# Kernel optimization log

Hardware: AMD Instinct MI355X
Metric: run time of the kernel (lower is better)

The kernel has to match this reference:

```python
import jax, jax.numpy as jnp
import numpy as np

B, N = 16384, 20
NODE_D, EDGE_D, TIME_D = 172, 172, 100
H = 2
OUT_D = NODE_D + TIME_D          # 272, pad_dim == 0
KEY_D = NODE_D + EDGE_D + TIME_D  # 444
HD = OUT_D // H                   # 136
LN_EPS = 1e-5


def setup_inputs() -> dict:
    key = jax.random.key(0)
    ks = jax.random.split(key, 12)
    s = lambda fan_in: 1.0 / np.sqrt(fan_in)
    return {
        "node_feat": jax.random.normal(ks[0], (B, NODE_D), jnp.float32),
        "time_feat": jax.random.normal(ks[1], (B, 1, TIME_D), jnp.float32),
        "nbr_node_feat": jax.random.normal(ks[2], (B, N, NODE_D), jnp.float32),
        "nbr_time_feat": jax.random.normal(ks[3], (B, N, TIME_D), jnp.float32),
        "nbr_edge_feat": jax.random.normal(ks[4], (B, N, EDGE_D), jnp.float32),
        "nbr_mask": jax.random.randint(ks[5], (B, N), 0, 2, jnp.int32),
        # linear weights, torch convention [out, in]
        "W_Q": jax.random.uniform(ks[6], (OUT_D, OUT_D), jnp.float32, -s(OUT_D), s(OUT_D)),
        "W_K": jax.random.uniform(ks[7], (OUT_D, KEY_D), jnp.float32, -s(KEY_D), s(KEY_D)),
        "W_V": jax.random.uniform(ks[8], (OUT_D, KEY_D), jnp.float32, -s(KEY_D), s(KEY_D)),
        "W_O": jax.random.uniform(ks[9], (OUT_D, OUT_D), jnp.float32, -s(OUT_D), s(OUT_D)),
        "b_O": jax.random.uniform(ks[10], (OUT_D,), jnp.float32, -s(OUT_D), s(OUT_D)),
        "ln_g": jnp.ones((OUT_D,), jnp.float32),
        "ln_b": jnp.zeros((OUT_D,), jnp.float32),
    }


def reference(node_feat, time_feat, nbr_node_feat, nbr_time_feat, nbr_edge_feat,
              nbr_mask, W_Q, W_K, W_V, W_O, b_O, ln_g, ln_b):
    # query: [B,1,OUT_D] = cat(node_feat, time_feat)
    q_in = jnp.concatenate([node_feat[:, None, :], time_feat], axis=2)
    residual = q_in
    # key/value input: [B,N,KEY_D]
    kv_in = jnp.concatenate([nbr_node_feat, nbr_edge_feat, nbr_time_feat], axis=2)

    Q = (q_in @ W_Q.T).reshape(B, 1, H, HD)   # bqhd
    K = (kv_in @ W_K.T).reshape(B, N, H, HD)  # bnhd
    V = (kv_in @ W_V.T).reshape(B, N, H, HD)

    scores = jnp.einsum('bqhd,bnhd->bhqn', Q, K) * (HD ** -0.5)  # [B,H,1,N]
    mask = (nbr_mask == 0)[:, None, None, :]                      # [B,1,1,N]
    scores = jnp.where(mask, jnp.float32(-1e10), scores)
    A = jax.nn.softmax(scores, axis=-1)  # dropout is identity (eval)

    O = jnp.einsum('bhqn,bnhd->bqhd', A, V).reshape(B, 1, OUT_D)
    out = O @ W_O.T + b_O
    x = out + residual
    mu = jnp.mean(x, axis=-1, keepdims=True)
    var = jnp.mean(jnp.square(x - mu), axis=-1, keepdims=True)
    x = (x - mu) * jax.lax.rsqrt(var + LN_EPS) * ln_g + ln_b
    return x[:, 0, :]  # [B, OUT_D]
```

## Files before the change

kernel.cpp:

```cpp
#include <hip/hip_runtime.h>


namespace {
constexpr int kB = 16384;
constexpr int kN = 20;
constexpr float kScale = 0.08574929257125441f;
constexpr float kLnEps = 1e-5f;

constexpr size_t kOffMsw = 0;
constexpr size_t kOffPsw = kOffMsw + 516096;
constexpr size_t kOffQT16 = kOffPsw + 487424;

constexpr int kMswBlocks = 56 * 9 * 8;
constexpr int kPswBlocks = 17 * 28 * 8;
}

typedef __attribute__((ext_vector_type(8))) short s8v;
typedef __attribute__((ext_vector_type(4))) float f4v;

__device__ __forceinline__ unsigned short f2bf(float x) {
  unsigned int u = __float_as_uint(x);
  unsigned int r = (u + 0x7FFFu + ((u >> 16) & 1u)) >> 16;
  return (unsigned short)r;
}
__device__ __forceinline__ float bf2f(unsigned short h) {
  return __uint_as_float(((unsigned int)h) << 16);
}
__device__ __forceinline__ float fma4(float4 a, float4 b, float acc) {
  acc = fmaf(a.x, b.x, acc);
  acc = fmaf(a.y, b.y, acc);
  acc = fmaf(a.z, b.z, acc);
  acc = fmaf(a.w, b.w, acc);
  return acc;
}
__device__ __forceinline__ s8v pack8(float4 lo, float4 hi) {
  s8v a;
  a[0] = (short)f2bf(lo.x); a[1] = (short)f2bf(lo.y);
  a[2] = (short)f2bf(lo.z); a[3] = (short)f2bf(lo.w);
  a[4] = (short)f2bf(hi.x); a[5] = (short)f2bf(hi.y);
  a[6] = (short)f2bf(hi.z); a[7] = (short)f2bf(hi.w);
  return a;
}

__device__ __forceinline__ float dpp_sum(float x) {
  int v = __float_as_int(x), t;
  t = __builtin_amdgcn_update_dpp(0, v, 0x111, 0xf, 0xf, true);
  v = __float_as_int(__int_as_float(v) + __int_as_float(t));
  t = __builtin_amdgcn_update_dpp(0, v, 0x112, 0xf, 0xf, true);
  v = __float_as_int(__int_as_float(v) + __int_as_float(t));
  t = __builtin_amdgcn_update_dpp(0, v, 0x114, 0xf, 0xf, true);
  v = __float_as_int(__int_as_float(v) + __int_as_float(t));
  t = __builtin_amdgcn_update_dpp(0, v, 0x118, 0xf, 0xf, true);
  v = __float_as_int(__int_as_float(v) + __int_as_float(t));
  t = __builtin_amdgcn_update_dpp(0, v, 0x142, 0xf, 0xf, true);
  v = __float_as_int(__int_as_float(v) + __int_as_float(t));
  t = __builtin_amdgcn_update_dpp(0, v, 0x143, 0xf, 0xf, true);
  v = __float_as_int(__int_as_float(v) + __int_as_float(t));
  return __int_as_float(v);
}
__device__ __forceinline__ float rdl63(float x) {
  return __int_as_float(__builtin_amdgcn_readlane(__float_as_int(x), 63));
}
__device__ __forceinline__ float rfl(float x) {
  return __int_as_float(__builtin_amdgcn_readfirstlane(__float_as_int(x)));
}

__global__ __launch_bounds__(64) void k_build_mp(const float* __restrict__ WQ,
                                                 const float* __restrict__ WK,
                                                 const float* __restrict__ WO,
                                                 const float* __restrict__ WV,
                                                 unsigned short* __restrict__ Msw,
                                                 unsigned short* __restrict__ Psw) {
  const int l = threadIdx.x;
  if (blockIdx.x < kMswBlocks) {
    const int bid = blockIdx.x;
    const int e = bid % 8;
    const int ks = (bid / 8) % 9;
    const int tile = bid / 72;
    const int jj = tile * 16 + (l & 15);
    const int h = jj / 448;
    const int j = jj - h * 448;
    const int i = ks * 32 + (l >> 4) * 8 + e;
    float s = 0.f;
    if (j < 444 && i < 272) {
      const float* wq = WQ + h * 136 * 272 + i;
      const float* wk = WK + h * 136 * 444 + j;
#pragma unroll 8
      for (int d = 0; d < 136; ++d) s = fmaf(wq[d * 272], wk[d * 444], s);
    }
    Msw[((size_t)(tile * 9 + ks) * 64 + l) * 8 + e] = f2bf(s);
  } else {
    const int bid = blockIdx.x - kMswBlocks;
    const int e = bid % 8;
    const int ks = (bid / 8) % 28;
    const int tile = bid / 224;
    const int n = tile * 16 + (l & 15);
    const int k = ks * 32 + (l >> 4) * 8 + e;
    const int h = k / 448;
    const int j = k - h * 448;
    float s = 0.f;
    if (j < 444) {
      const float* wo = WO + (size_t)n * 272 + h * 136;
      const float* wv = WV + h * 136 * 444 + j;
#pragma unroll 8
      for (int d = 0; d < 136; ++d) s = fmaf(wo[d], wv[d * 444], s);
    }
    Psw[((size_t)(tile * 28 + ks) * 64 + l) * 8 + e] = f2bf(s);
  }
}

__global__ __launch_bounds__(256) void k_gemm_a(const float* __restrict__ node,
                                                const float* __restrict__ timef,
                                                const unsigned short* __restrict__ Msw,
                                                unsigned short* __restrict__ QT16) {
  const int tid = threadIdx.x;
  const int l = tid & 63, w = tid >> 6;
  const int m0 = blockIdx.x * 16;
  const int mrow = m0 + (l & 15);
  const int koff = (l >> 4) * 8;
  const float4* n4 = reinterpret_cast<const float4*>(node + (size_t)mrow * 172);
  const float4* t4 = reinterpret_cast<const float4*>(timef + (size_t)mrow * 100);
  const float4 z4 = make_float4(0.f, 0.f, 0.f, 0.f);
  f4v acc[14];
#pragma unroll
  for (int t = 0; t < 14; ++t) acc[t] = (f4v){0.f, 0.f, 0.f, 0.f};
  for (int ks = 0; ks < 9; ++ks) {
    const int c0 = ks * 32 + koff;
    float4 lo = z4, hi = z4;
    if (c0 + 8 <= 172) {
      lo = n4[c0 / 4];
      hi = n4[c0 / 4 + 1];
    } else if (c0 == 168) {
      lo = n4[42];
      hi = t4[0];
    } else if (c0 + 8 <= 272) {
      lo = t4[(c0 - 172) / 4];
      hi = t4[(c0 - 172) / 4 + 1];
    }
    const s8v a = pack8(lo, hi);
    const unsigned short* bp = Msw + ((size_t)(w * 14) * 9 + ks) * 64 * 8 + (size_t)l * 8;
#pragma unroll
    for (int t = 0; t < 14; ++t) {
      const s8v b = *reinterpret_cast<const s8v*>(bp + (size_t)t * 9 * 64 * 8);
      acc[t] = __builtin_amdgcn_mfma_f32_16x16x32_bf16(a, b, acc[t], 0, 0, 0);
    }
  }
  const int r0 = (l >> 4) * 4;
#pragma unroll
  for (int t = 0; t < 14; ++t) {
    const int n = (w * 14 + t) * 16 + (l & 15);
#pragma unroll
    for (int r = 0; r < 4; ++r)
      QT16[(size_t)(m0 + r0 + r) * 896 + n] = f2bf(acc[t][r]);
  }
}

__global__ __launch_bounds__(256) void k_attn(const float* __restrict__ nnode,
                                              const float* __restrict__ nedge,
                                              const float* __restrict__ ntime,
                                              const int* __restrict__ mask,
                                              unsigned short* __restrict__ QT16) {
  const int l = threadIdx.x & 63;
  const int w = threadIdx.x >> 6;
  const int b = blockIdx.x * 4 + w;
  const bool v1 = (l < 47);
  const float4* nnode4 = reinterpret_cast<const float4*>(nnode);
  const float4* nedge4 = reinterpret_cast<const float4*>(nedge);
  const float4* ntime4 = reinterpret_cast<const float4*>(ntime);
  const float4 z4 = make_float4(0.f, 0.f, 0.f, 0.f);
  unsigned short* qrow = QT16 + (size_t)b * 896;
  const int* mrow = mask + (size_t)b * kN;

  auto ldq = [&](int so) {
    const ushort4 u = *reinterpret_cast<const ushort4*>(qrow + so);
    return make_float4(bf2f(u.x), bf2f(u.y), bf2f(u.z), bf2f(u.w));
  };
  const float4 q00 = ldq(4 * l);
  const float4 q01 = v1 ? ldq(256 + 4 * l) : z4;
  const float4 q10 = ldq(448 + 4 * l);
  const float4 q11 = v1 ? ldq(448 + 256 + 4 * l) : z4;

  unsigned mbits = 0;
#pragma unroll
  for (int n = 0; n < kN; ++n) mbits |= (mrow[n] != 0 ? 1u : 0u) << n;

  auto ldkv = [&](int n, float4& k0, float4& k1) {
    const size_t row = (size_t)b * kN + n;
    k0 = (l < 43) ? nnode4[row * 43 + l] : nedge4[row * 43 + (l - 43)];
    k1 = z4;
    if (v1) {
      const int j4 = 64 + l;
      k1 = (j4 < 86) ? nedge4[row * 43 + (j4 - 43)] : ntime4[row * 25 + (j4 - 86)];
    }
  };

  float4 va00 = z4, va01 = z4, va10 = z4, va11 = z4;
  float i0, i1;

  if (mbits == 0u) {
#pragma unroll 1
    for (int n = 0; n < kN; ++n) {
      float4 kv0, kv1;
      ldkv(n, kv0, kv1);
      va00.x += kv0.x; va00.y += kv0.y; va00.z += kv0.z; va00.w += kv0.w;
      va01.x += kv1.x; va01.y += kv1.y; va01.z += kv1.z; va01.w += kv1.w;
    }
    va10 = va00;
    va11 = va01;
    i0 = 1.0f / 20.0f;
    i1 = 1.0f / 20.0f;
  } else {
    float m0 = -1e30f, m1 = -1e30f, l0 = 0.f, l1 = 0.f;
#pragma unroll
    for (int n = 0; n < kN; ++n) {
      if (!(mbits & (1u << n))) continue;
      float4 kv0, kv1;
      ldkv(n, kv0, kv1);
      float ps0 = fma4(q01, kv1, fma4(q00, kv0, 0.f));
      float ps1 = fma4(q11, kv1, fma4(q10, kv0, 0.f));
      const float sa0 = rdl63(dpp_sum(ps0));
      const float sa1 = rdl63(dpp_sum(ps1));
      const float s0 = sa0 * kScale;
      const float s1 = sa1 * kScale;
      {
        const float mn = fmaxf(m0, s0);
        const float al = __expf(m0 - mn);
        const float p = __expf(s0 - mn);
        l0 = l0 * al + p;
        m0 = mn;
        va00.x = fmaf(p, kv0.x, va00.x * al);
        va00.y = fmaf(p, kv0.y, va00.y * al);
        va00.z = fmaf(p, kv0.z, va00.z * al);
        va00.w = fmaf(p, kv0.w, va00.w * al);
        va01.x = fmaf(p, kv1.x, va01.x * al);
        va01.y = fmaf(p, kv1.y, va01.y * al);
        va01.z = fmaf(p, kv1.z, va01.z * al);
        va01.w = fmaf(p, kv1.w, va01.w * al);
      }
      {
        const float mn = fmaxf(m1, s1);
        const float al = __expf(m1 - mn);
        const float p = __expf(s1 - mn);
        l1 = l1 * al + p;
        m1 = mn;
        va10.x = fmaf(p, kv0.x, va10.x * al);
        va10.y = fmaf(p, kv0.y, va10.y * al);
        va10.z = fmaf(p, kv0.z, va10.z * al);
        va10.w = fmaf(p, kv0.w, va10.w * al);
        va11.x = fmaf(p, kv1.x, va11.x * al);
        va11.y = fmaf(p, kv1.y, va11.y * al);
        va11.z = fmaf(p, kv1.z, va11.z * al);
        va11.w = fmaf(p, kv1.w, va11.w * al);
      }
    }
    i0 = rfl(1.0f / l0);
    i1 = rfl(1.0f / l1);
  }

  auto stq = [&](int so, float4 v, float s) {
    ushort4 u;
    u.x = f2bf(v.x * s); u.y = f2bf(v.y * s); u.z = f2bf(v.z * s); u.w = f2bf(v.w * s);
    *reinterpret_cast<ushort4*>(qrow + so) = u;
  };
  stq(4 * l, va00, i0);
  if (v1) stq(256 + 4 * l, va01, i0);
  stq(448 + 4 * l, va10, i1);
  if (v1) stq(448 + 256 + 4 * l, va11, i1);
}

__global__ __launch_bounds__(256) void k_out_mfma(const unsigned short* __restrict__ VT16,
                                                  const unsigned short* __restrict__ Psw,
                                                  const float* __restrict__ node,
                                                  const float* __restrict__ timef,
                                                  const float* __restrict__ bO,
                                                  const float* __restrict__ g,
                                                  const float* __restrict__ be,
                                                  float* __restrict__ out) {
  __shared__ float xl[16][273];
  const int tid = threadIdx.x;
  const int l = tid & 63, w = tid >> 6;
  const int m0 = blockIdx.x * 16;
  const int mrow = m0 + (l & 15);
  const int koff = (l >> 4) * 8;
  f4v acc[5];
#pragma unroll
  for (int i = 0; i < 5; ++i) acc[i] = (f4v){0.f, 0.f, 0.f, 0.f};
  for (int ks = 0; ks < 28; ++ks) {
    const s8v a = *reinterpret_cast<const s8v*>(VT16 + (size_t)mrow * 896 + ks * 32 + koff);
#pragma unroll
    for (int i = 0; i < 5; ++i) {
      const int t = w + 4 * i;
      if (t < 17) {
        const s8v bfr = *reinterpret_cast<const s8v*>(Psw + ((size_t)(t * 28 + ks) * 64 + l) * 8);
        acc[i] = __builtin_amdgcn_mfma_f32_16x16x32_bf16(a, bfr, acc[i], 0, 0, 0);
      }
    }
  }
  const int r0 = (l >> 4) * 4;
#pragma unroll
  for (int i = 0; i < 5; ++i) {
    const int t = w + 4 * i;
    if (t < 17) {
#pragma unroll
      for (int r = 0; r < 4; ++r) xl[r0 + r][t * 16 + (l & 15)] = acc[i][r];
    }
  }
  __syncthreads();
  for (int bb = w; bb < 16; bb += 4) {
    const int b = m0 + bb;
    float v[5];
    float sum = 0.f, sq = 0.f;
#pragma unroll
    for (int k = 0; k < 5; ++k) {
      const int o = l + 64 * k;
      v[k] = 0.f;
      if (o < 272) {
        const float r = (o < 172) ? node[(size_t)b * 172 + o] : timef[(size_t)b * 100 + (o - 172)];
        const float x = xl[bb][o] + bO[o] + r;
        v[k] = x;
        sum += x;
        sq = fmaf(x, x, sq);
      }
    }
#pragma unroll
    for (int off = 32; off >= 1; off >>= 1) {
      sum += __shfl_xor(sum, off, 64);
      sq += __shfl_xor(sq, off, 64);
    }
    const float mu = sum * (1.0f / 272.0f);
    const float var = sq * (1.0f / 272.0f) - mu * mu;
    const float rs = rsqrtf(var + kLnEps);
#pragma unroll
    for (int k = 0; k < 5; ++k) {
      const int o = l + 64 * k;
      if (o < 272) out[(size_t)b * 272 + o] = (v[k] - mu) * rs * g[o] + be[o];
    }
  }
}

extern "C" void kernel_launch(void* const* d_in, const int* in_sizes, int n_in,
                              void* d_out, int out_size, void* d_ws, size_t ws_size,
                              hipStream_t stream) {
  const float* node = (const float*)d_in[0];
  const float* timef = (const float*)d_in[1];
  const float* nnode = (const float*)d_in[2];
  const float* ntime = (const float*)d_in[3];
  const float* nedge = (const float*)d_in[4];
  const int* mask = (const int*)d_in[5];
  const float* WQ = (const float*)d_in[6];
  const float* WK = (const float*)d_in[7];
  const float* WV = (const float*)d_in[8];
  const float* WO = (const float*)d_in[9];
  const float* bO = (const float*)d_in[10];
  const float* g = (const float*)d_in[11];
  const float* be = (const float*)d_in[12];

  char* ws = (char*)d_ws;
  unsigned short* Msw = (unsigned short*)(ws + kOffMsw);
  unsigned short* Psw = (unsigned short*)(ws + kOffPsw);
  unsigned short* QT16 = (unsigned short*)(ws + kOffQT16);
  float* out = (float*)d_out;

  hipLaunchKernelGGL(k_build_mp, dim3(kMswBlocks + kPswBlocks), dim3(64), 0, stream,
                     WQ, WK, WO, WV, Msw, Psw);
  hipLaunchKernelGGL(k_gemm_a, dim3(kB / 16), dim3(256), 0, stream, node, timef, Msw, QT16);
  hipLaunchKernelGGL(k_attn, dim3(kB / 4), dim3(256), 0, stream, nnode, nedge, ntime, mask, QT16);
  hipLaunchKernelGGL(k_out_mfma, dim3(kB / 16), dim3(256), 0, stream, QT16, Psw, node, timef, bO, g, be, out);
}
```

Baseline: 193.0 us.

## Fuse query GEMM, attention and output GEMM+LayerNorm into one kernel via LDS

Merges the three per-batch kernels (query projection GEMM, attention over neighbours, output projection plus LayerNorm) into a single 1024-thread kernel that handles 16 rows per block. The intermediate 896-wide bf16 row stays in shared memory instead of making a round trip through global workspace, and two launches are removed. MFMA tiles are redistributed across 16 waves, so each wave does less GEMM work but the output GEMM leaves waves idle (17 tiles over 16 waves). LDS use (~29KB) and 1024-thread blocks may limit occupancy and latency hiding in the memory-bound attention phase.

```diff
diff --git a/kernel.cpp b/kernel.cpp
--- a/kernel.cpp
+++ b/kernel.cpp
@@ -6,10 +6,10 @@
 constexpr int kN = 20;
 constexpr float kScale = 0.08574929257125441f;
 constexpr float kLnEps = 1e-5f;
+constexpr int kQS = 904;
 
 constexpr size_t kOffMsw = 0;
 constexpr size_t kOffPsw = kOffMsw + 516096;
-constexpr size_t kOffQT16 = kOffPsw + 487424;
 
 constexpr int kMswBlocks = 56 * 9 * 8;
 constexpr int kPswBlocks = 17 * 28 * 8;
@@ -109,205 +109,205 @@
   }
 }
 
-__global__ __launch_bounds__(256) void k_gemm_a(const float* __restrict__ node,
-                                                const float* __restrict__ timef,
-                                                const unsigned short* __restrict__ Msw,
-                                                unsigned short* __restrict__ QT16) {
+__global__ __launch_bounds__(1024, 8) void k_fused(const float* __restrict__ node,
+                                                   const float* __restrict__ timef,
+                                                   const float* __restrict__ nnode,
+                                                   const float* __restrict__ nedge,
+                                                   const float* __restrict__ ntime,
+                                                   const int* __restrict__ mask,
+                                                   const unsigned short* __restrict__ Msw,
+                                                   const unsigned short* __restrict__ Psw,
+                                                   const float* __restrict__ bO,
+                                                   const float* __restrict__ g,
+                                                   const float* __restrict__ be,
+                                                   float* __restrict__ out) {
+  __shared__ unsigned short qlds[16 * kQS];
   const int tid = threadIdx.x;
   const int l = tid & 63, w = tid >> 6;
   const int m0 = blockIdx.x * 16;
-  const int mrow = m0 + (l & 15);
-  const int koff = (l >> 4) * 8;
-  const float4* n4 = reinterpret_cast<const float4*>(node + (size_t)mrow * 172);
-  const float4* t4 = reinterpret_cast<const float4*>(timef + (size_t)mrow * 100);
   const float4 z4 = make_float4(0.f, 0.f, 0.f, 0.f);
-  f4v acc[14];
-#pragma unroll
-  for (int t = 0; t < 14; ++t) acc[t] = (f4v){0.f, 0.f, 0.f, 0.f};
-  for (int ks = 0; ks < 9; ++ks) {
-    const int c0 = ks * 32 + koff;
-    float4 lo = z4, hi = z4;
-    if (c0 + 8 <= 172) {
-      lo = n4[c0 / 4];
-      hi = n4[c0 / 4 + 1];
-    } else if (c0 == 168) {
-      lo = n4[42];
-      hi = t4[0];
-    } else if (c0 + 8 <= 272) {
-      lo = t4[(c0 - 172) / 4];
-      hi = t4[(c0 - 172) / 4 + 1];
-    }
-    const s8v a = pack8(lo, hi);
-    const unsigned short* bp = Msw + ((size_t)(w * 14) * 9 + ks) * 64 * 8 + (size_t)l * 8;
-#pragma unroll
-    for (int t = 0; t < 14; ++t) {
-      const s8v b = *reinterpret_cast<const s8v*>(bp + (size_t)t * 9 * 64 * 8);
-      acc[t] = __builtin_amdgcn_mfma_f32_16x16x32_bf16(a, b, acc[t], 0, 0, 0);
-    }
-  }
-  const int r0 = (l >> 4) * 4;
-#pragma unroll
-  for (int t = 0; t < 14; ++t) {
-    const int n = (w * 14 + t) * 16 + (l & 15);
-#pragma unroll
-    for (int r = 0; r < 4; ++r)
-      QT16[(size_t)(m0 + r0 + r) * 896 + n] = f2bf(acc[t][r]);
-  }
-}
-
-__global__ __launch_bounds__(256) void k_attn(const float* __restrict__ nnode,
-                                              const float* __restrict__ nedge,
-                                              const float* __restrict__ ntime,
-                                              const int* __restrict__ mask,
-                                              unsigned short* __restrict__ QT16) {
-  const int l = threadIdx.x & 63;
-  const int w = threadIdx.x >> 6;
-  const int b = blockIdx.x * 4 + w;
-  const bool v1 = (l < 47);
-  const float4* nnode4 = reinterpret_cast<const float4*>(nnode);
-  const float4* nedge4 = reinterpret_cast<const float4*>(nedge);
-  const float4* ntime4 = reinterpret_cast<const float4*>(ntime);
-  const float4 z4 = make_float4(0.f, 0.f, 0.f, 0.f);
-  unsigned short* qrow = QT16 + (size_t)b * 896;
-  const int* mrow = mask + (size_t)b * kN;
-
-  auto ldq = [&](int so) {
-    const ushort4 u = *reinterpret_cast<const ushort4*>(qrow + so);
-    return make_float4(bf2f(u.x), bf2f(u.y), bf2f(u.z), bf2f(u.w));
-  };
-  const float4 q00 = ldq(4 * l);
-  const float4 q01 = v1 ? ldq(256 + 4 * l) : z4;
-  const float4 q10 = ldq(448 + 4 * l);
-  const float4 q11 = v1 ? ldq(448 + 256 + 4 * l) : z4;
-
-  unsigned mbits = 0;
-#pragma unroll
-  for (int n = 0; n < kN; ++n) mbits |= (mrow[n] != 0 ? 1u : 0u) << n;
-
-  auto ldkv = [&](int n, float4& k0, float4& k1) {
-    const size_t row = (size_t)b * kN + n;
-    k0 = (l < 43) ? nnode4[row * 43 + l] : nedge4[row * 43 + (l - 43)];
-    k1 = z4;
-    if (v1) {
-      const int j4 = 64 + l;
-      k1 = (j4 < 86) ? nedge4[row * 43 + (j4 - 43)] : ntime4[row * 25 + (j4 - 86)];
-    }
-  };
-
-  float4 va00 = z4, va01 = z4, va10 = z4, va11 = z4;
-  float i0, i1;
-
-  if (mbits == 0u) {
-#pragma unroll 1
-    for (int n = 0; n < kN; ++n) {
-      float4 kv0, kv1;
-      ldkv(n, kv0, kv1);
-      va00.x += kv0.x; va00.y += kv0.y; va00.z += kv0.z; va00.w += kv0.w;
-      va01.x += kv1.x; va01.y += kv1.y; va01.z += kv1.z; va01.w += kv1.w;
-    }
-    va10 = va00;
-    va11 = va01;
-    i0 = 1.0f / 20.0f;
-    i1 = 1.0f / 20.0f;
-  } else {
-    float m0 = -1e30f, m1 = -1e30f, l0 = 0.f, l1 = 0.f;
-#pragma unroll
-    for (int n = 0; n < kN; ++n) {
-      if (!(mbits & (1u << n))) continue;
-      float4 kv0, kv1;
-      ldkv(n, kv0, kv1);
-      float ps0 = fma4(q01, kv1, fma4(q00, kv0, 0.f));
-      float ps1 = fma4(q11, kv1, fma4(q10, kv0, 0.f));
-      const float sa0 = rdl63(dpp_sum(ps0));
-      const float sa1 = rdl63(dpp_sum(ps1));
-      const float s0 = sa0 * kScale;
-      const float s1 = sa1 * kScale;
-      {
-        const float mn = fmaxf(m0, s0);
-        const float al = __expf(m0 - mn);
-        const float p = __expf(s0 - mn);
-        l0 = l0 * al + p;
-        m0 = mn;
-        va00.x = fmaf(p, kv0.x, va00.x * al);
-        va00.y = fmaf(p, kv0.y, va00.y * al);
-        va00.z = fmaf(p, kv0.z, va00.z * al);
-        va00.w = fmaf(p, kv0.w, va00.w * al);
-        va01.x = fmaf(p, kv1.x, va01.x * al);
-        va01.y = fmaf(p, kv1.y, va01.y * al);
-        va01.z = fmaf(p, kv1.z, va01.z * al);
-        va01.w = fmaf(p, kv1.w, va01.w * al);
-      }
-      {
-        const float mn = fmaxf(m1, s1);
-        const float al = __expf(m1 - mn);
-        const float p = __expf(s1 - mn);
-        l1 = l1 * al + p;
-        m1 = mn;
-        va10.x = fmaf(p, kv0.x, va10.x * al);
-        va10.y = fmaf(p, kv0.y, va10.y * al);
-        va10.z = fmaf(p, kv0.z, va10.z * al);
-        va10.w = fmaf(p, kv0.w, va10.w * al);
-        va11.x = fmaf(p, kv1.x, va11.x * al);
-        va11.y = fmaf(p, kv1.y, va11.y * al);
-        va11.z = fmaf(p, kv1.z, va11.z * al);
-        va11.w = fmaf(p, kv1.w, va11.w * al);
-      }
-    }
-    i0 = rfl(1.0f / l0);
-    i1 = rfl(1.0f / l1);
-  }
-
-  auto stq = [&](int so, float4 v, float s) {
-    ushort4 u;
-    u.x = f2bf(v.x * s); u.y = f2bf(v.y * s); u.z = f2bf(v.z * s); u.w = f2bf(v.w * s);
-    *reinterpret_cast<ushort4*>(qrow + so) = u;
-  };
-  stq(4 * l, va00, i0);
-  if (v1) stq(256 + 4 * l, va01, i0);
-  stq(448 + 4 * l, va10, i1);
-  if (v1) stq(448 + 256 + 4 * l, va11, i1);
-}
-
-__global__ __launch_bounds__(256) void k_out_mfma(const unsigned short* __restrict__ VT16,
-                                                  const unsigned short* __restrict__ Psw,
-                                                  const float* __restrict__ node,
-                                                  const float* __restrict__ timef,
-                                                  const float* __restrict__ bO,
-                                                  const float* __restrict__ g,
-                                                  const float* __restrict__ be,
-                                                  float* __restrict__ out) {
-  __shared__ float xl[16][273];
-  const int tid = threadIdx.x;
-  const int l = tid & 63, w = tid >> 6;
-  const int m0 = blockIdx.x * 16;
-  const int mrow = m0 + (l & 15);
-  const int koff = (l >> 4) * 8;
-  f4v acc[5];
-#pragma unroll
-  for (int i = 0; i < 5; ++i) acc[i] = (f4v){0.f, 0.f, 0.f, 0.f};
-  for (int ks = 0; ks < 28; ++ks) {
-    const s8v a = *reinterpret_cast<const s8v*>(VT16 + (size_t)mrow * 896 + ks * 32 + koff);
-#pragma unroll
-    for (int i = 0; i < 5; ++i) {
-      const int t = w + 4 * i;
-      if (t < 17) {
-        const s8v bfr = *reinterpret_cast<const s8v*>(Psw + ((size_t)(t * 28 + ks) * 64 + l) * 8);
-        acc[i] = __builtin_amdgcn_mfma_f32_16x16x32_bf16(a, bfr, acc[i], 0, 0, 0);
-      }
-    }
-  }
-  const int r0 = (l >> 4) * 4;
-#pragma unroll
-  for (int i = 0; i < 5; ++i) {
-    const int t = w + 4 * i;
-    if (t < 17) {
-#pragma unroll
-      for (int r = 0; r < 4; ++r) xl[r0 + r][t * 16 + (l & 15)] = acc[i][r];
+
+  {
+    const int mrow = m0 + (l & 15);
+    const int koff = (l >> 4) * 8;
+    const float4* n4 = reinterpret_cast<const float4*>(node + (size_t)mrow * 172);
+    const float4* t4 = reinterpret_cast<const float4*>(timef + (size_t)mrow * 100);
+    f4v acc[4];
+#pragma unroll
+    for (int i = 0; i < 4; ++i) acc[i] = (f4v){0.f, 0.f, 0.f, 0.f};
+    for (int ks = 0; ks < 9; ++ks) {
+      const int c0 = ks * 32 + koff;
+      float4 lo = z4, hi = z4;
+      if (c0 + 8 <= 172) {
+        lo = n4[c0 / 4];
+        hi = n4[c0 / 4 + 1];
+      } else if (c0 == 168) {
+        lo = n4[42];
+        hi = t4[0];
+      } else if (c0 + 8 <= 272) {
+        lo = t4[(c0 - 172) / 4];
+        hi = t4[(c0 - 172) / 4 + 1];
+      }
+      const s8v a = pack8(lo, hi);
+#pragma unroll
+      for (int i = 0; i < 4; ++i) {
+        const int t = w + 16 * i;
+        if (t < 56) {
+          const s8v b = *reinterpret_cast<const s8v*>(Msw + ((size_t)(t * 9 + ks) * 64 + l) * 8);
+          acc[i] = __builtin_amdgcn_mfma_f32_16x16x32_bf16(a, b, acc[i], 0, 0, 0);
+        }
+      }
+    }
+    const int r0 = (l >> 4) * 4;
+#pragma unroll
+    for (int i = 0; i < 4; ++i) {
+      const int t = w + 16 * i;
+      if (t < 56) {
+        const int n = t * 16 + (l & 15);
+#pragma unroll
+        for (int r = 0; r < 4; ++r) qlds[(size_t)(r0 + r) * kQS + n] = f2bf(acc[i][r]);
+      }
     }
   }
   __syncthreads();
-  for (int bb = w; bb < 16; bb += 4) {
-    const int b = m0 + bb;
+
+  {
+    const int b = m0 + w;
+    const bool v1 = (l < 47);
+    const float4* nnode4 = reinterpret_cast<const float4*>(nnode);
+    const float4* nedge4 = reinterpret_cast<const float4*>(nedge);
+    const float4* ntime4 = reinterpret_cast<const float4*>(ntime);
+    unsigned short* qrow = qlds + (size_t)w * kQS;
+    const int* mrow = mask + (size_t)b * kN;
+
+    auto ldq = [&](int so) {
+      const ushort4 u = *reinterpret_cast<const ushort4*>(qrow + so);
+      return make_float4(bf2f(u.x), bf2f(u.y), bf2f(u.z), bf2f(u.w));
+    };
+    const float4 q00 = ldq(4 * l);
+    const float4 q01 = v1 ? ldq(256 + 4 * l) : z4;
+    const float4 q10 = ldq(448 + 4 * l);
+    const float4 q11 = v1 ? ldq(448 + 256 + 4 * l) : z4;
+
+    unsigned mbits = 0;
+#pragma unroll
+    for (int n = 0; n < kN; ++n) mbits |= (mrow[n] != 0 ? 1u : 0u) << n;
+
+    auto ldkv = [&](int n, float4& k0, float4& k1) {
+      const size_t row = (size_t)b * kN + n;
+      k0 = (l < 43) ? nnode4[row * 43 + l] : nedge4[row * 43 + (l - 43)];
+      k1 = z4;
+      if (v1) {
+        const int j4 = 64 + l;
+        k1 = (j4 < 86) ? nedge4[row * 43 + (j4 - 43)] : ntime4[row * 25 + (j4 - 86)];
+      }
+    };
+
+    float4 va00 = z4, va01 = z4, va10 = z4, va11 = z4;
+    float i0, i1;
+
+    if (mbits == 0u) {
+#pragma unroll 1
+      for (int n = 0; n < kN; ++n) {
+        float4 kv0, kv1;
+        ldkv(n, kv0, kv1);
+        va00.x += kv0.x; va00.y += kv0.y; va00.z += kv0.z; va00.w += kv0.w;
+        va01.x += kv1.x; va01.y += kv1.y; va01.z += kv1.z; va01.w += kv1.w;
+      }
+      va10 = va00;
+      va11 = va01;
+      i0 = 1.0f / 20.0f;
+      i1 = 1.0f / 20.0f;
+    } else {
+      float m0s = -1e30f, m1s = -1e30f, l0 = 0.f, l1 = 0.f;
+#pragma unroll
+      for (int n = 0; n < kN; ++n) {
+        if (!(mbits & (1u << n))) continue;
+        float4 kv0, kv1;
+        ldkv(n, kv0, kv1);
+        float ps0 = fma4(q01, kv1, fma4(q00, kv0, 0.f));
+        float ps1 = fma4(q11, kv1, fma4(q10, kv0, 0.f));
+        const float sa0 = rdl63(dpp_sum(ps0));
+        const float sa1 = rdl63(dpp_sum(ps1));
+        const float s0 = sa0 * kScale;
+        const float s1 = sa1 * kScale;
+        {
+          const float mn = fmaxf(m0s, s0);
+          const float al = __expf(m0s - mn);
+          const float p = __expf(s0 - mn);
+          l0 = l0 * al + p;
+          m0s = mn;
+          va00.x = fmaf(p, kv0.x, va00.x * al);
+          va00.y = fmaf(p, kv0.y, va00.y * al);
+          va00.z = fmaf(p, kv0.z, va00.z * al);
+          va00.w = fmaf(p, kv0.w, va00.w * al);
+          va01.x = fmaf(p, kv1.x, va01.x * al);
+          va01.y = fmaf(p, kv1.y, va01.y * al);
+          va01.z = fmaf(p, kv1.z, va01.z * al);
+          va01.w = fmaf(p, kv1.w, va01.w * al);
+        }
+        {
+          const float mn = fmaxf(m1s, s1);
+          const float al = __expf(m1s - mn);
+          const float p = __expf(s1 - mn);
+          l1 = l1 * al + p;
+          m1s = mn;
+          va10.x = fmaf(p, kv0.x, va10.x * al);
+          va10.y = fmaf(p, kv0.y, va10.y * al);
+          va10.z = fmaf(p, kv0.z, va10.z * al);
+          va10.w = fmaf(p, kv0.w, va10.w * al);
+          va11.x = fmaf(p, kv1.x, va11.x * al);
+          va11.y = fmaf(p, kv1.y, va11.y * al);
+          va11.z = fmaf(p, kv1.z, va11.z * al);
+          va11.w = fmaf(p, kv1.w, va11.w * al);
+        }
+      }
+      i0 = rfl(1.0f / l0);
+      i1 = rfl(1.0f / l1);
+    }
+
+    auto stq = [&](int so, float4 v, float s) {
+      ushort4 u;
+      u.x = f2bf(v.x * s); u.y = f2bf(v.y * s); u.z = f2bf(v.z * s); u.w = f2bf(v.w * s);
+      *reinterpret_cast<ushort4*>(qrow + so) = u;
+    };
+    stq(4 * l, va00, i0);
+    if (v1) stq(256 + 4 * l, va01, i0);
+    stq(448 + 4 * l, va10, i1);
+    if (v1) stq(448 + 256 + 4 * l, va11, i1);
+  }
+  __syncthreads();
+
+  {
+    const int koff = (l >> 4) * 8;
+    f4v acc[2];
+    acc[0] = (f4v){0.f, 0.f, 0.f, 0.f};
+    acc[1] = (f4v){0.f, 0.f, 0.f, 0.f};
+    for (int ks = 0; ks < 28; ++ks) {
+      const s8v aA = *reinterpret_cast<const s8v*>(qlds + (size_t)(l & 15) * kQS + ks * 32 + koff);
+#pragma unroll
+      for (int i = 0; i < 2; ++i) {
+        const int t = w + 16 * i;
+        if (t < 17) {
+          const s8v bfr = *reinterpret_cast<const s8v*>(Psw + ((size_t)(t * 28 + ks) * 64 + l) * 8);
+          acc[i] = __builtin_amdgcn_mfma_f32_16x16x32_bf16(aA, bfr, acc[i], 0, 0, 0);
+        }
+      }
+    }
+    __syncthreads();
+    float* xl = reinterpret_cast<float*>(qlds);
+    const int r0 = (l >> 4) * 4;
+#pragma unroll
+    for (int i = 0; i < 2; ++i) {
+      const int t = w + 16 * i;
+      if (t < 17) {
+#pragma unroll
+        for (int r = 0; r < 4; ++r)
+          xl[(size_t)(r0 + r) * 273 + t * 16 + (l & 15)] = acc[i][r];
+      }
+    }
+    __syncthreads();
+    const int b = m0 + w;
     float v[5];
     float sum = 0.f, sq = 0.f;
 #pragma unroll
@@ -316,7 +316,7 @@
       v[k] = 0.f;
       if (o < 272) {
         const float r = (o < 172) ? node[(size_t)b * 172 + o] : timef[(size_t)b * 100 + (o - 172)];
-        const float x = xl[bb][o] + bO[o] + r;
+        const float x = xl[(size_t)w * 273 + o] + bO[o] + r;
         v[k] = x;
         sum += x;
         sq = fmaf(x, x, sq);
@@ -358,12 +358,10 @@
   char* ws = (char*)d_ws;
   unsigned short* Msw = (unsigned short*)(ws + kOffMsw);
   unsigned short* Psw = (unsigned short*)(ws + kOffPsw);
-  unsigned short* QT16 = (unsigned short*)(ws + kOffQT16);
   float* out = (float*)d_out;
 
   hipLaunchKernelGGL(k_build_mp, dim3(kMswBlocks + kPswBlocks), dim3(64), 0, stream,
                      WQ, WK, WO, WV, Msw, Psw);
-  hipLaunchKernelGGL(k_gemm_a, dim3(kB / 16), dim3(256), 0, stream, node, timef, Msw, QT16);
-  hipLaunchKernelGGL(k_attn, dim3(kB / 4), dim3(256), 0, stream, nnode, nedge, ntime, mask, QT16);
-  hipLaunchKernelGGL(k_out_mfma, dim3(kB / 16), dim3(256), 0, stream, QT16, Psw, node, timef, bO, g, be, out);
-}
+  hipLaunchKernelGGL(k_fused, dim3(kB / 16), dim3(1024), 0, stream,
+                     node, timef, nnode, nedge, ntime, mask, Msw, Psw, bO, g, be, out);
+}
```

After: 174.4 us (median of 2 runs). 9.6% less time.
